# Performance work log

Hardware: AMD Instinct MI355X
Metric: run time of the kernel (lower is better)

## Reference

```python
import jax, jax.numpy as jnp
import numpy as np

N = 65536       # active voxels
C = 128         # embed_channels
DEPTH = 4
NSEG = 1024     # number of clusters per level
K = 27          # 3x3x3 kernel taps
LRELU = 0.01
EPS_BN = 1e-5


def _bn(x, g, b):
    # training-mode batchnorm over the voxel axis (biased variance, as torch)
    m = jnp.mean(x, axis=0)
    v = jnp.var(x, axis=0)
    return (x - m) * jax.lax.rsqrt(v + EPS_BN) * g + b


def _lrelu(x):
    return jnp.where(x >= 0, x, LRELU * x)


def _proj(x, w, g, b):
    # Linear(bias=False) -> BatchNorm1d -> LeakyReLU
    return _lrelu(_bn(x @ w, g, b))


def setup_inputs() -> dict:
    key = jax.random.key(0)
    ks = jax.random.split(key, 24)
    s = 1.0 / np.sqrt(C)
    sc = 1.0 / np.sqrt(K * C)
    u = lambda k, shp, sk: jax.random.uniform(k, shp, jnp.float32, -sk, sk)
    g = lambda k, shp: 1.0 + 0.1 * jax.random.normal(k, shp, jnp.float32)
    inp = {}
    inp['feat'] = jax.random.normal(ks[0], (N, C), jnp.float32)
    inp['clusters'] = jax.random.randint(ks[1], (DEPTH - 1, N), 0, NSEG)
    # neighbor table for 3x3x3 sparse conv; value == N means neighbor absent
    inp['neighbor_idx'] = jax.random.randint(ks[2], (N, K), 0, N + 1)
    inp['lw_w'] = u(ks[3], (DEPTH - 1, C, C), s)
    inp['lw_gamma'] = g(ks[4], (DEPTH - 1, C))
    inp['lw_beta'] = 0.1 * jax.random.normal(ks[5], (DEPTH - 1, C), jnp.float32)
    inp['w_w'] = u(ks[6], (DEPTH - 1, C, C), s)
    inp['proj_w'] = u(ks[7], (DEPTH, C, C), s)
    inp['proj_gamma'] = g(ks[8], (DEPTH, C))
    inp['proj_beta'] = 0.1 * jax.random.normal(ks[9], (DEPTH, C), jnp.float32)
    inp['adaptive_w'] = u(ks[10], (C, DEPTH - 1), s)
    inp['fuse_w'] = u(ks[11], (2 * C, C), 1.0 / np.sqrt(2 * C))
    inp['fuse_gamma'] = g(ks[12], (C,))
    inp['fuse_beta'] = 0.1 * jax.random.normal(ks[13], (C,), jnp.float32)
    inp['conv1_w'] = u(ks[14], (K, C, C), sc)
    inp['conv2_w'] = u(ks[15], (K, C, C), sc)
    inp['bn1_gamma'] = g(ks[16], (C,))
    inp['bn1_beta'] = 0.1 * jax.random.normal(ks[17], (C,), jnp.float32)
    inp['bn2_gamma'] = g(ks[18], (C,))
    inp['bn2_beta'] = 0.1 * jax.random.normal(ks[19], (C,), jnp.float32)
    return inp


def _forward(feat, clusters, neighbor_idx, lw_w, lw_gamma, lw_beta, w_w,
             proj_w, proj_gamma, proj_beta, adaptive_w, fuse_w, fuse_gamma,
             fuse_beta, conv1_w, conv2_w, bn1_gamma, bn1_beta, bn2_gamma,
             bn2_beta):
    x_in = feat
    feats = []
    for i in range(DEPTH - 1):
        c = clusters[i]
        pw = _proj(feat, lw_w[i], lw_gamma[i], lw_beta[i])          # [N,C]
        cnt = jnp.maximum(
            jax.ops.segment_sum(jnp.ones((N,), feat.dtype), c, num_segments=NSEG), 1.0)
        seg_mean = jax.ops.segment_sum(pw, c, num_segments=NSEG) / cnt[:, None]
        pw = pw - seg_mean[c]                                        # center per cluster
        pw = pw @ w_w[i]
        pw = jnp.exp(pw - jnp.max(pw))                               # global max, as in source
        pw = pw / (jax.ops.segment_sum(pw, c, num_segments=NSEG)[c] + 1e-6)
        pf = _proj(feat, proj_w[i], proj_gamma[i], proj_beta[i]) * pw
        feats.append(jax.ops.segment_sum(pf, c, num_segments=NSEG)[c])
    adp = jax.nn.softmax(feat @ adaptive_w, axis=1)                  # [N,3]
    feats = jnp.stack(feats, axis=1)                                 # [N,3,C]
    agg = jnp.einsum('ld,ldc->lc', adp, feats)                       # [N,C]
    f_last = _proj(feat, proj_w[DEPTH - 1], proj_gamma[DEPTH - 1], proj_beta[DEPTH - 1])
    fused = _proj(jnp.concatenate([f_last, agg], axis=1), fuse_w, fuse_gamma, fuse_beta) + x_in
    residual = fused
    # 3x3x3 sparse conv on fixed topology: 27 masked gathers + per-tap GEMM
    mask = (neighbor_idx < N).astype(fused.dtype)                    # [N,K]
    idx = jnp.minimum(neighbor_idx, N - 1)

    def sconv(x, w):
        out = jnp.zeros((N, C), x.dtype)
        for k in range(K):
            out = out + (jnp.take(x, idx[:, k], axis=0) * mask[:, k:k + 1]) @ w[k]
        return out

    d = _lrelu(_bn(sconv(fused, conv1_w), bn1_gamma, bn1_beta))
    d = _lrelu(_bn(sconv(d, conv2_w), bn2_gamma, bn2_beta) + residual)
    return d


def reference(feat, clusters, neighbor_idx, lw_w, lw_gamma, lw_beta, w_w,
              proj_w, proj_gamma, proj_beta, adaptive_w, fuse_w, fuse_gamma,
              fuse_beta, conv1_w, conv2_w, bn1_gamma, bn1_beta, bn2_gamma,
              bn2_beta):
    return _forward(feat, clusters, neighbor_idx, lw_w, lw_gamma, lw_beta,
                    w_w, proj_w, proj_gamma, proj_beta, adaptive_w, fuse_w,
                    fuse_gamma, fuse_beta, conv1_w, conv2_w, bn1_gamma,
                    bn1_beta, bn2_gamma, bn2_beta)
```

## Files before the change

kernel.cpp:

```cpp
#include <hip/hip_runtime.h>

typedef unsigned short u16;
typedef unsigned int u32;
typedef __attribute__((ext_vector_type(8))) short bf16x8;
typedef __attribute__((ext_vector_type(4))) float f32x4;
typedef __attribute__((ext_vector_type(4))) u32 u32x4;

#define NROWS 65536
#define CCH 128
#define PE ((size_t)65537*128)

__device__ __forceinline__ float bf2f(u16 x){ u32 u=((u32)x)<<16; return __builtin_bit_cast(float,u); }
__device__ __forceinline__ u16 f2bf(float f){ u32 u=__builtin_bit_cast(u32,f); u += 0x7fffu + ((u>>16)&1u); return (u16)(u>>16); }
__device__ __forceinline__ float lrelu(float v){ return v>=0.f? v : 0.01f*v; }
__device__ __forceinline__ u32 fenc(float f){ u32 u=__builtin_bit_cast(u32,f); return (u & 0x80000000u) ? ~u : (u | 0x80000000u); }
__device__ __forceinline__ float fdec(u32 u){ u32 b = (u & 0x80000000u) ? (u ^ 0x80000000u) : ~u; return __builtin_bit_cast(float,b); }

__global__ __launch_bounds__(256) void prep_transpose(
    const float* __restrict__ lw, const float* __restrict__ ww, const float* __restrict__ pj,
    const float* __restrict__ fw, const float* __restrict__ c1, const float* __restrict__ c2,
    u16* __restrict__ WT)
{
  int i = blockIdx.x*256 + threadIdx.x;
  float v;
  if (i < 49152)      { int j=i;        int m=j>>14,e=j&16383,n=e>>7,k=e&127; v=lw[(m<<14)+(k<<7)+n]; }
  else if (i < 98304) { int j=i-49152;  int m=j>>14,e=j&16383,n=e>>7,k=e&127; v=ww[(m<<14)+(k<<7)+n]; }
  else if (i < 163840){ int j=i-98304;  int m=j>>14,e=j&16383,n=e>>7,k=e&127; v=pj[(m<<14)+(k<<7)+n]; }
  else if (i < 196608){ int j=i-163840; int n=j>>8, k=j&255;                  v=fw[(k<<7)+n]; }
  else if (i < 638976){ int j=i-196608; int m=j>>14,e=j&16383,n=e>>7,k=e&127; v=c1[(m<<14)+(k<<7)+n]; }
  else                { int j=i-638976; int m=j>>14,e=j&16383,n=e>>7,k=e&127; v=c2[(m<<14)+(k<<7)+n]; }
  WT[i]=f2bf(v);
}

__global__ __launch_bounds__(256) void nbrT_k(const int* __restrict__ nbr, int* __restrict__ nbrT){
  __shared__ int s[64*27];
  int b = blockIdx.x;
  for (int i=threadIdx.x; i<64*27; i+=256) s[i] = nbr[b*64*27 + i];
  __syncthreads();
  for (int i=threadIdx.x; i<64*27; i+=256){
    int tap=i>>6, row=i&63;
    nbrT[(size_t)tap*NROWS + b*64 + row] = s[row*27 + tap];
  }
}

__global__ __launch_bounds__(256) void hist_k(const int* __restrict__ cl, int* __restrict__ cnt){
  int i = blockIdx.x*256 + threadIdx.x;
  int l = i>>16;
  atomicAdd(&cnt[l*1024 + cl[i]], 1);
}
__global__ __launch_bounds__(1024) void scan_k(const int* __restrict__ cnt, int* __restrict__ starts, int* __restrict__ cur){
  int l = blockIdx.x, t = threadIdx.x;
  __shared__ int s[1024];
  int v = cnt[l*1024+t];
  s[t]=v; __syncthreads();
  for (int off=1; off<1024; off<<=1){
    int u_ = (t>=off) ? s[t-off] : 0;
    __syncthreads();
    s[t] += u_;
    __syncthreads();
  }
  int incl=s[t], excl=incl-v;
  starts[l*1025+t]=excl;
  if (t==1023) starts[l*1025+1024]=incl;
  cur[l*1024+t]=excl;
}
__global__ __launch_bounds__(256) void scatter_k(const int* __restrict__ cl, int* __restrict__ cur, int* __restrict__ order){
  int i = blockIdx.x*256 + threadIdx.x;
  int l = i>>16;
  int c = cl[i];
  int p = atomicAdd(&cur[l*1024+c], 1);
  order[l*65536 + p] = i & 65535;
}

struct BS7 { const u16* BT[7]; u16* out[7]; float* stats[7]; };

__global__ __launch_bounds__(256,2) void gemm_feat7(const float* __restrict__ feat, BS7 p)
{
  const int tid=threadIdx.x, lane=tid&63, quad=lane>>4, l15=lane&15;
  const int w=tid>>6, rh=w>>1, chq=w&1;
  const int row0=blockIdx.x*128;

  __shared__ __align__(16) u16 ldsA[128*136];
  __shared__ float cs[256];

  #pragma unroll
  for (int it=0; it<8; ++it){
    int row = it*16 + (tid>>4), chn = tid&15;
    const float* Af = feat + (size_t)(row0+row)*CCH + chn*8;
    float4 lo = *(const float4*)(Af);
    float4 hi = *(const float4*)(Af+4);
    u32x4 d;
    d[0]=(u32)f2bf(lo.x)|((u32)f2bf(lo.y)<<16);
    d[1]=(u32)f2bf(lo.z)|((u32)f2bf(lo.w)<<16);
    d[2]=(u32)f2bf(hi.x)|((u32)f2bf(hi.y)<<16);
    d[3]=(u32)f2bf(hi.z)|((u32)f2bf(hi.w)<<16);
    *(u32x4*)(&ldsA[row*136 + chn*8]) = d;
  }
  __syncthreads();

  #pragma unroll 1
  for (int y=0; y<7; ++y){
    const u16* Bb = p.BT[y];
    f32x4 acc[4][4];
    #pragma unroll
    for (int a_=0;a_<4;++a_)
      #pragma unroll
      for (int b_=0;b_<4;++b_) acc[a_][b_]=(f32x4){0.f,0.f,0.f,0.f};
    #pragma unroll
    for (int ks=0; ks<4; ++ks){
      bf16x8 af[4], bfv[4];
      #pragma unroll
      for (int mb=0;mb<4;++mb)
        af[mb]=*(const bf16x8*)(&ldsA[(rh*64+mb*16+l15)*136 + ks*32 + quad*8]);
      #pragma unroll
      for (int nb=0;nb<4;++nb)
        bfv[nb]=*(const bf16x8*)(Bb + (size_t)(chq*64+nb*16+l15)*CCH + ks*32 + quad*8);
      #pragma unroll
      for (int mb=0;mb<4;++mb)
        #pragma unroll
        for (int nb=0;nb<4;++nb)
          acc[mb][nb]=__builtin_amdgcn_mfma_f32_16x16x32_bf16(af[mb],bfv[nb],acc[mb][nb],0,0,0);
    }
    u16* O = p.out[y];
    #pragma unroll
    for (int mb=0;mb<4;++mb){
      int rbase=row0+rh*64+mb*16+quad*4;
      #pragma unroll
      for (int e=0;e<4;++e)
        #pragma unroll
        for (int nb=0;nb<4;++nb)
          O[(size_t)(rbase+e)*CCH + chq*64+nb*16+l15]=f2bf(acc[mb][nb][e]);
    }
    __syncthreads();
    cs[tid]=0.f;
    __syncthreads();
    #pragma unroll
    for (int nb=0;nb<4;++nb){
      float s=0.f,s2=0.f;
      #pragma unroll
      for (int mb=0;mb<4;++mb)
        #pragma unroll
        for (int e=0;e<4;++e){ float v=acc[mb][nb][e]; s+=v; s2+=v*v; }
      s += __shfl_xor(s,16);  s += __shfl_xor(s,32);
      s2+= __shfl_xor(s2,16); s2+= __shfl_xor(s2,32);
      if (lane<16){
        int col=chq*64+nb*16+l15;
        atomicAdd(&cs[col],s); atomicAdd(&cs[128+col],s2);
      }
    }
    __syncthreads();
    atomicAdd(&p.stats[y][tid], cs[tid]);
  }
}

struct BS3 { const u16* A[3]; const u16* BT[3]; float* out[3]; u32* gmax[3]; };

__global__ __launch_bounds__(256,2) void gemm_w3(BS3 p)
{
  const int tid=threadIdx.x, lane=tid&63, quad=lane>>4, l15=lane&15;
  const int w=tid>>6, rh=w>>1, chq=w&1;
  const int row0=blockIdx.x*128;
  const int y=blockIdx.y;

  __shared__ __align__(16) u16 ldsA[128*136];
  __shared__ float wred[4];

  const u16* A = p.A[y];
  #pragma unroll
  for (int it=0; it<8; ++it){
    int row = it*16 + (tid>>4), chn = tid&15;
    *(u32x4*)(&ldsA[row*136 + chn*8]) = *(const u32x4*)(A + (size_t)(row0+row)*CCH + chn*8);
  }
  __syncthreads();

  const u16* Bb = p.BT[y];
  f32x4 acc[4][4];
  #pragma unroll
  for (int a_=0;a_<4;++a_)
    #pragma unroll
    for (int b_=0;b_<4;++b_) acc[a_][b_]=(f32x4){0.f,0.f,0.f,0.f};
  #pragma unroll
  for (int ks=0; ks<4; ++ks){
    bf16x8 af[4], bfv[4];
    #pragma unroll
    for (int mb=0;mb<4;++mb)
      af[mb]=*(const bf16x8*)(&ldsA[(rh*64+mb*16+l15)*136 + ks*32 + quad*8]);
    #pragma unroll
    for (int nb=0;nb<4;++nb)
      bfv[nb]=*(const bf16x8*)(Bb + (size_t)(chq*64+nb*16+l15)*CCH + ks*32 + quad*8);
    #pragma unroll
    for (int mb=0;mb<4;++mb)
      #pragma unroll
      for (int nb=0;nb<4;++nb)
        acc[mb][nb]=__builtin_amdgcn_mfma_f32_16x16x32_bf16(af[mb],bfv[nb],acc[mb][nb],0,0,0);
  }
  float* O = p.out[y];
  float m=-3.0e38f;
  #pragma unroll
  for (int mb=0;mb<4;++mb){
    int rbase=row0+rh*64+mb*16+quad*4;
    #pragma unroll
    for (int e=0;e<4;++e)
      #pragma unroll
      for (int nb=0;nb<4;++nb){
        float v=acc[mb][nb][e];
        O[(size_t)(rbase+e)*CCH + chq*64+nb*16+l15]=v;
        m=fmaxf(m,v);
      }
  }
  #pragma unroll
  for (int o=1;o<64;o<<=1) m=fmaxf(m,__shfl_xor(m,o));
  if (lane==0) wred[w]=m;
  __syncthreads();
  if (tid==0){
    float mm=fmaxf(fmaxf(wred[0],wred[1]),fmaxf(wred[2],wred[3]));
    atomicMax(p.gmax[y], fenc(mm));
  }
}

__global__ __launch_bounds__(256,2) void gemm_fuse(
    const u16* __restrict__ A0, const u16* __restrict__ A1,
    const float* __restrict__ tstat, const float* __restrict__ tg, const float* __restrict__ tb,
    const u16* __restrict__ BT, u16* __restrict__ out, float* __restrict__ stats)
{
  const int tid=threadIdx.x, lane=tid&63, quad=lane>>4, l15=lane&15;
  const int w=tid>>6, rh=w>>1, chq=w&1;
  const int row0=blockIdx.x*128;

  __shared__ __align__(16) u16 ldsA[128*136];
  __shared__ float tsc[128], tsh[128];
  __shared__ float cs[256];

  if (tid<128){
    float s=tstat[tid], s2=tstat[128+tid];
    float mean=s*(1.0f/65536.0f);
    float var =s2*(1.0f/65536.0f)-mean*mean;
    float rstd=rsqrtf(var+1e-5f);
    float scv =tg[tid]*rstd;
    tsc[tid]=scv; tsh[tid]=tb[tid]-mean*scv;
  }

  f32x4 acc[4][4];
  #pragma unroll
  for (int a_=0;a_<4;++a_)
    #pragma unroll
    for (int b_=0;b_<4;++b_) acc[a_][b_]=(f32x4){0.f,0.f,0.f,0.f};

  #pragma unroll 1
  for (int tap=0; tap<2; ++tap){
    __syncthreads();
    const u16* Ab = tap ? A1 : A0;
    #pragma unroll
    for (int it=0; it<8; ++it){
      int row = it*16 + (tid>>4), chn = tid&15;
      u32x4 d = *(const u32x4*)(Ab + (size_t)(row0+row)*CCH + chn*8);
      if (tap==0){
        #pragma unroll
        for (int pq=0;pq<4;++pq){
          u32 xv=d[pq]; int k=chn*8+2*pq;
          float f0=lrelu(tsc[k  ]*bf2f((u16)(xv&0xffffu))+tsh[k  ]);
          float f1=lrelu(tsc[k+1]*bf2f((u16)(xv>>16))    +tsh[k+1]);
          d[pq]=(u32)f2bf(f0)|((u32)f2bf(f1)<<16);
        }
      }
      *(u32x4*)(&ldsA[row*136 + chn*8]) = d;
    }
    __syncthreads();
    const u16* Bb = BT + tap*128;
    #pragma unroll
    for (int ks=0; ks<4; ++ks){
      bf16x8 af[4], bfv[4];
      #pragma unroll
      for (int mb=0;mb<4;++mb)
        af[mb]=*(const bf16x8*)(&ldsA[(rh*64+mb*16+l15)*136 + ks*32 + quad*8]);
      #pragma unroll
      for (int nb=0;nb<4;++nb)
        bfv[nb]=*(const bf16x8*)(Bb + (size_t)(chq*64+nb*16+l15)*256 + ks*32 + quad*8);
      #pragma unroll
      for (int mb=0;mb<4;++mb)
        #pragma unroll
        for (int nb=0;nb<4;++nb)
          acc[mb][nb]=__builtin_amdgcn_mfma_f32_16x16x32_bf16(af[mb],bfv[nb],acc[mb][nb],0,0,0);
    }
  }
  #pragma unroll
  for (int mb=0;mb<4;++mb){
    int rbase=row0+rh*64+mb*16+quad*4;
    #pragma unroll
    for (int e=0;e<4;++e)
      #pragma unroll
      for (int nb=0;nb<4;++nb)
        out[(size_t)(rbase+e)*CCH + chq*64+nb*16+l15]=f2bf(acc[mb][nb][e]);
  }
  __syncthreads();
  cs[tid]=0.f;
  __syncthreads();
  #pragma unroll
  for (int nb=0;nb<4;++nb){
    float s=0.f,s2=0.f;
    #pragma unroll
    for (int mb=0;mb<4;++mb)
      #pragma unroll
      for (int e=0;e<4;++e){ float v=acc[mb][nb][e]; s+=v; s2+=v*v; }
    s += __shfl_xor(s,16);  s += __shfl_xor(s,32);
    s2+= __shfl_xor(s2,16); s2+= __shfl_xor(s2,32);
    if (lane<16){
      int col=chq*64+nb*16+l15;
      atomicAdd(&cs[col],s); atomicAdd(&cs[128+col],s2);
    }
  }
  __syncthreads();
  atomicAdd(&stats[tid], cs[tid]);
}

__global__ __launch_bounds__(256,2) void conv_k(
    const u16* __restrict__ A, const u16* __restrict__ BT,
    const int* __restrict__ nbrT, u16* __restrict__ out, float* __restrict__ stats)
{
  const int tid=threadIdx.x, lane=tid&63, quad=lane>>4, l15=lane&15;
  const int w=tid>>6, rh=w>>1, chq=w&1;
  const int row0=blockIdx.x*128;
  const int srow=tid>>4, schn=tid&15;

  __shared__ __align__(16) u16 bufA[2][128*136];
  __shared__ float cs[256];

  u32x4 pre[8];
  int idxn[8];
  #pragma unroll
  for (int it=0; it<8; ++it){
    int arow = nbrT[row0 + it*16 + srow];
    pre[it] = *(const u32x4*)(A + (size_t)arow*CCH + schn*8);
  }
  #pragma unroll
  for (int it=0; it<8; ++it)
    idxn[it] = nbrT[(size_t)NROWS + row0 + it*16 + srow];
  #pragma unroll
  for (int it=0; it<8; ++it)
    *(u32x4*)(&bufA[0][(it*16+srow)*136 + schn*8]) = pre[it];
  __syncthreads();

  f32x4 acc[4][4];
  #pragma unroll
  for (int a_=0;a_<4;++a_)
    #pragma unroll
    for (int b_=0;b_<4;++b_) acc[a_][b_]=(f32x4){0.f,0.f,0.f,0.f};

  #pragma unroll 1
  for (int tap=0; tap<27; ++tap){
    const int cur = tap&1, nxt = cur^1;
    if (tap<26){
      #pragma unroll
      for (int it=0; it<8; ++it)
        pre[it] = *(const u32x4*)(A + (size_t)idxn[it]*CCH + schn*8);
      if (tap<25){
        #pragma unroll
        for (int it=0; it<8; ++it)
          idxn[it] = nbrT[(size_t)(tap+2)*NROWS + row0 + it*16 + srow];
      }
    }
    const u16* Bb = BT + tap*16384;
    #pragma unroll
    for (int ks=0; ks<4; ++ks){
      bf16x8 af[4], bfv[4];
      #pragma unroll
      for (int mb=0;mb<4;++mb)
        af[mb]=*(const bf16x8*)(&bufA[cur][(rh*64+mb*16+l15)*136 + ks*32 + quad*8]);
      #pragma unroll
      for (int nb=0;nb<4;++nb)
        bfv[nb]=*(const bf16x8*)(Bb + (size_t)(chq*64+nb*16+l15)*CCH + ks*32 + quad*8);
      #pragma unroll
      for (int mb=0;mb<4;++mb)
        #pragma unroll
        for (int nb=0;nb<4;++nb)
          acc[mb][nb]=__builtin_amdgcn_mfma_f32_16x16x32_bf16(af[mb],bfv[nb],acc[mb][nb],0,0,0);
    }
    if (tap<26){
      #pragma unroll
      for (int it=0; it<8; ++it)
        *(u32x4*)(&bufA[nxt][(it*16+srow)*136 + schn*8]) = pre[it];
    }
    __syncthreads();
  }

  #pragma unroll
  for (int mb=0;mb<4;++mb){
    int rbase=row0+rh*64+mb*16+quad*4;
    #pragma unroll
    for (int e=0;e<4;++e)
      #pragma unroll
      for (int nb=0;nb<4;++nb)
        out[(size_t)(rbase+e)*CCH + chq*64+nb*16+l15]=f2bf(acc[mb][nb][e]);
  }
  cs[tid]=0.f;
  __syncthreads();
  #pragma unroll
  for (int nb=0;nb<4;++nb){
    float s=0.f,s2=0.f;
    #pragma unroll
    for (int mb=0;mb<4;++mb)
      #pragma unroll
      for (int e=0;e<4;++e){ float v=acc[mb][nb][e]; s+=v; s2+=v*v; }
    s += __shfl_xor(s,16);  s += __shfl_xor(s,32);
    s2+= __shfl_xor(s2,16); s2+= __shfl_xor(s2,32);
    if (lane<16){
      int col=chq*64+nb*16+l15;
      atomicAdd(&cs[col],s); atomicAdd(&cs[128+col],s2);
    }
  }
  __syncthreads();
  atomicAdd(&stats[tid], cs[tid]);
}

__global__ __launch_bounds__(256) void seg_bn_center_all(
    u16* __restrict__ pbase, const float* __restrict__ stats,
    const float* __restrict__ gamma, const float* __restrict__ beta,
    const int* __restrict__ starts, const int* __restrict__ order)
{
  __shared__ float sc[128], sh[128], ssum[128], smean[128];
  const int tid=threadIdx.x, b=blockIdx.x;
  const int level=b>>10, seg=b&1023;
  u16* praw = pbase + (size_t)level*PE;
  const float* st = stats + level*256;
  if (tid<128){
    float s=st[tid], s2=st[128+tid];
    float mean=s*(1.0f/65536.0f);
    float var =s2*(1.0f/65536.0f)-mean*mean;
    float rstd=rsqrtf(var+1e-5f);
    float scv =gamma[level*128+tid]*rstd;
    sc[tid]=scv; sh[tid]=beta[level*128+tid]-mean*scv;
    ssum[tid]=0.f;
  }
  __syncthreads();
  const int s0=starts[level*1025+seg], en=starts[level*1025+seg+1];
  const int c2=tid&63, half=tid>>6;
  const int* ord = order + level*65536;
  const float sc0=sc[2*c2], sc1=sc[2*c2+1], sh0=sh[2*c2], sh1=sh[2*c2+1];
  float a0=0.f, a1=0.f;
  for (int m=s0+half; m<en; m+=4){
    int r=ord[m];
    u32 x=*(const u32*)(praw + (size_t)r*CCH + 2*c2);
    a0 += lrelu(sc0*bf2f((u16)(x&0xffffu))+sh0);
    a1 += lrelu(sc1*bf2f((u16)(x>>16))    +sh1);
  }
  atomicAdd(&ssum[2*c2],a0); atomicAdd(&ssum[2*c2+1],a1);
  __syncthreads();
  if (tid<128) smean[tid]=ssum[tid]/fmaxf((float)(en-s0),1.0f);
  __syncthreads();
  const float m0=smean[2*c2], m1=smean[2*c2+1];
  for (int m=s0+half; m<en; m+=4){
    int r=ord[m];
    u32 x=*(const u32*)(praw + (size_t)r*CCH + 2*c2);
    float v0=lrelu(sc0*bf2f((u16)(x&0xffffu))+sh0)-m0;
    float v1=lrelu(sc1*bf2f((u16)(x>>16))    +sh1)-m1;
    *(u32*)(praw + (size_t)r*CCH + 2*c2) = (u32)f2bf(v0)|((u32)f2bf(v1)<<16);
  }
}

struct F3 { const float* f[3]; };
__global__ __launch_bounds__(256) void seg_softmax_all(
    F3 pw2s, const u16* __restrict__ pfbase,
    const float* __restrict__ stats, const float* __restrict__ gamma, const float* __restrict__ beta,
    const u32* __restrict__ gmax,
    const int* __restrict__ starts, const int* __restrict__ order,
    float* __restrict__ segpf)
{
  __shared__ float sc[128], sh[128], se[128], spf[128];
  const int tid=threadIdx.x, b=blockIdx.x;
  const int level=b>>10, seg=b&1023;
  const float* pw2 = pw2s.f[level];
  const u16* pfraw = pfbase + (size_t)level*PE;
  const float* st = stats + level*256;
  if (tid<128){
    float s=st[tid], s2=st[128+tid];
    float mean=s*(1.0f/65536.0f);
    float var =s2*(1.0f/65536.0f)-mean*mean;
    float rstd=rsqrtf(var+1e-5f);
    float scv =gamma[level*128+tid]*rstd;
    sc[tid]=scv; sh[tid]=beta[level*128+tid]-mean*scv;
    se[tid]=0.f; spf[tid]=0.f;
  }
  __syncthreads();
  const float M = fdec(gmax[level]);
  const int s0=starts[level*1025+seg], en=starts[level*1025+seg+1];
  const int c2=tid&63, half=tid>>6;
  const int* ord = order + level*65536;
  float a0=0.f, a1=0.f;
  for (int m=s0+half; m<en; m+=4){
    int r=ord[m];
    float2 x=*(const float2*)(pw2 + (size_t)r*CCH + 2*c2);
    a0 += __expf(x.x-M); a1 += __expf(x.y-M);
  }
  atomicAdd(&se[2*c2],a0); atomicAdd(&se[2*c2+1],a1);
  __syncthreads();
  const float d0=1.0f/(se[2*c2]+1e-6f), d1=1.0f/(se[2*c2+1]+1e-6f);
  const float sc0=sc[2*c2], sc1=sc[2*c2+1], sh0=sh[2*c2], sh1=sh[2*c2+1];
  float p0=0.f, p1=0.f;
  for (int m=s0+half; m<en; m+=4){
    int r=ord[m];
    float2 x=*(const float2*)(pw2 + (size_t)r*CCH + 2*c2);
    u32 f=*(const u32*)(pfraw + (size_t)r*CCH + 2*c2);
    p0 += lrelu(sc0*bf2f((u16)(f&0xffffu))+sh0) * (__expf(x.x-M)*d0);
    p1 += lrelu(sc1*bf2f((u16)(f>>16))    +sh1) * (__expf(x.y-M)*d1);
  }
  atomicAdd(&spf[2*c2],p0); atomicAdd(&spf[2*c2+1],p1);
  __syncthreads();
  if (tid<128) segpf[(size_t)b*128+tid]=spf[tid];
}

__global__ __launch_bounds__(256) void adp_agg(
    const float* __restrict__ feat, const float* __restrict__ aw,
    const int* __restrict__ clusters, const float* __restrict__ segpf,
    u16* __restrict__ agg)
{
  const int tid=threadIdx.x, w=tid>>6, lane=tid&63;
  const int r = blockIdx.x*4 + w;
  float t0=0.f,t1=0.f,t2=0.f;
  #pragma unroll
  for (int cc=0; cc<2; ++cc){
    int c = lane + cc*64;
    float f=feat[(size_t)r*CCH+c];
    t0 += f*aw[c*3+0];
    t1 += f*aw[c*3+1];
    t2 += f*aw[c*3+2];
  }
  #pragma unroll
  for (int o=1;o<64;o<<=1){
    t0+=__shfl_xor(t0,o); t1+=__shfl_xor(t1,o); t2+=__shfl_xor(t2,o);
  }
  float m=fmaxf(t0,fmaxf(t1,t2));
  float e0=__expf(t0-m), e1=__expf(t1-m), e2=__expf(t2-m);
  float inv=1.0f/(e0+e1+e2);
  float p0=e0*inv,p1=e1*inv,p2=e2*inv;
  int c0=clusters[r], c1_=clusters[NROWS+r], c2_=clusters[2*NROWS+r];
  const float* s0p=segpf + (size_t)c0*128;
  const float* s1p=segpf + (size_t)(1024+c1_)*128;
  const float* s2p=segpf + (size_t)(2048+c2_)*128;
  #pragma unroll
  for (int cc=0; cc<2; ++cc){
    int c = lane + cc*64;
    float v = p0*s0p[c] + p1*s1p[c] + p2*s2p[c];
    agg[(size_t)r*CCH+c]=f2bf(v);
  }
}

__global__ __launch_bounds__(256) void apply_kernel(
    const u16* __restrict__ raw, const float* __restrict__ stats,
    const float* __restrict__ g_, const float* __restrict__ b_,
    const void* __restrict__ resid, int rf32,
    void* __restrict__ out, int of32,
    int nrows, int mode)
{
  __shared__ float sc[128], sh[128];
  const int tid=threadIdx.x;
  if (tid<128){
    float s=stats[tid], s2=stats[128+tid];
    float mean=s*(1.0f/65536.0f);
    float var =s2*(1.0f/65536.0f)-mean*mean;
    float rstd=rsqrtf(var+1e-5f);
    float scv =g_[tid]*rstd;
    sc[tid]=scv; sh[tid]=b_[tid]-mean*scv;
  }
  __syncthreads();
  size_t chunk = (size_t)blockIdx.x*256 + tid;
  size_t total = (size_t)nrows*16;
  if (chunk >= total) return;
  size_t r = chunk>>4; int c8 = (int)(chunk&15)*8;
  float v[8];
  if (r >= NROWS){
    #pragma unroll
    for (int p=0;p<8;++p) v[p]=0.f;
  } else {
    u32x4 x = *(const u32x4*)(raw + r*CCH + c8);
    float rsd[8];
    if (resid){
      if (rf32){
        const float* R = ((const float*)resid) + r*CCH + c8;
        float4 lo=*(const float4*)R, hi=*(const float4*)(R+4);
        rsd[0]=lo.x; rsd[1]=lo.y; rsd[2]=lo.z; rsd[3]=lo.w;
        rsd[4]=hi.x; rsd[5]=hi.y; rsd[6]=hi.z; rsd[7]=hi.w;
      } else {
        u32x4 rv = *(const u32x4*)(((const u16*)resid) + r*CCH + c8);
        #pragma unroll
        for (int p=0;p<4;++p){
          rsd[2*p]  =bf2f((u16)(rv[p]&0xffffu));
          rsd[2*p+1]=bf2f((u16)(rv[p]>>16));
        }
      }
    } else {
      #pragma unroll
      for (int p=0;p<8;++p) rsd[p]=0.f;
    }
    #pragma unroll
    for (int p=0;p<4;++p){
      u32 xv=x[p];
      int k=c8+2*p;
      float v0=sc[k  ]*bf2f((u16)(xv&0xffffu))+sh[k  ];
      float v1=sc[k+1]*bf2f((u16)(xv>>16))    +sh[k+1];
      if (mode==0){ v[2*p]=lrelu(v0)+rsd[2*p]; v[2*p+1]=lrelu(v1)+rsd[2*p+1]; }
      else        { v[2*p]=lrelu(v0+rsd[2*p]); v[2*p+1]=lrelu(v1+rsd[2*p+1]); }
    }
  }
  if (of32){
    float* O = ((float*)out) + r*CCH + c8;
    float4 lo={v[0],v[1],v[2],v[3]}, hi={v[4],v[5],v[6],v[7]};
    *(float4*)O = lo; *(float4*)(O+4) = hi;
  } else {
    u32x4 o;
    #pragma unroll
    for (int p=0;p<4;++p) o[p] = (u32)f2bf(v[2*p]) | ((u32)f2bf(v[2*p+1])<<16);
    *(u32x4*)(((u16*)out) + r*CCH + c8) = o;
  }
}

extern "C" void kernel_launch(void* const* d_in, const int* in_sizes, int n_in,
                              void* d_out, int out_size, void* d_ws, size_t ws_size,
                              hipStream_t stream)
{
  (void)in_sizes; (void)n_in; (void)out_size; (void)ws_size;
  const float* feat = (const float*)d_in[0];
  const int* clusters = (const int*)d_in[1];
  const int* nbr  = (const int*)d_in[2];
  const float* lw_w = (const float*)d_in[3];
  const float* lw_g = (const float*)d_in[4];
  const float* lw_b = (const float*)d_in[5];
  const float* w_w  = (const float*)d_in[6];
  const float* pj_w = (const float*)d_in[7];
  const float* pj_g = (const float*)d_in[8];
  const float* pj_b = (const float*)d_in[9];
  const float* aw   = (const float*)d_in[10];
  const float* fu_w = (const float*)d_in[11];
  const float* fu_g = (const float*)d_in[12];
  const float* fu_b = (const float*)d_in[13];
  const float* c1w  = (const float*)d_in[14];
  const float* c2w  = (const float*)d_in[15];
  const float* b1g  = (const float*)d_in[16];
  const float* b1b  = (const float*)d_in[17];
  const float* b2g  = (const float*)d_in[18];
  const float* b2b  = (const float*)d_in[19];

  char* wsb = (char*)d_ws;
  u16* WT = (u16*)wsb;
  const size_t o_zero = 2162688;
  float* stats = (float*)(wsb + o_zero);
  u32*  gmax   = (u32*) (wsb + o_zero + 10240);
  int*  cnt    = (int*) (wsb + o_zero + 10496);
  int*  cur    = (int*) (wsb + o_zero + 22784);
  float* segpf = (float*)(wsb + o_zero + 35072);
  const size_t zero_bytes = 35072 + (size_t)3*1024*128*4;
  const size_t o_starts = o_zero + 1607936;
  int* starts = (int*)(wsb + o_starts);
  const size_t o_order = o_starts + 12544;
  int* order  = (int*)(wsb + o_order);
  const size_t o_pool = o_order + 786432;
  const size_t PE_B = PE*2;
  u16* A0=(u16*)(wsb+o_pool + 0*PE_B);
  u16* A1=(u16*)(wsb+o_pool + 1*PE_B);
  u16* A2=(u16*)(wsb+o_pool + 2*PE_B);
  u16* A3=(u16*)(wsb+o_pool + 3*PE_B);
  u16* A4=(u16*)(wsb+o_pool + 4*PE_B);
  u16* A5=(u16*)(wsb+o_pool + 5*PE_B);
  u16* A6=(u16*)(wsb+o_pool + 6*PE_B);
  const size_t o_F = o_pool + 7*PE_B;
  float* F0=(float*)(wsb+o_F);
  float* F1=(float*)(wsb+o_F+33554432);
  float* F2=(float*)d_out;
  int* nbrT = (int*)(wsb+o_F);

  hipMemsetAsync(wsb+o_zero, 0, zero_bytes, stream);
  prep_transpose<<<4224,256,0,stream>>>(lw_w,w_w,pj_w,fu_w,c1w,c2w,WT);
  hist_k   <<<768,256,0,stream>>>(clusters, cnt);
  scan_k   <<<3,1024,0,stream>>>(cnt, starts, cur);
  scatter_k<<<768,256,0,stream>>>(clusters, cur, order);

  const u16* lwT = WT;
  const u16* wwT = WT + 49152;
  const u16* pjT = WT + 98304;
  const u16* fuT = WT + 163840;
  const u16* c1T = WT + 196608;
  const u16* c2T = WT + 638976;

  float* stLW=stats;
  float* stPJ=stats+768;
  float* stFU=stats+1792; float* stB1=stats+2048; float* stB2=stats+2304;

  {
    BS7 p;
    for (int i=0;i<3;++i){ p.BT[i]=lwT+i*16384;     p.out[i]=A0+(size_t)i*PE; p.stats[i]=stLW+i*256; }
    for (int i=0;i<4;++i){ p.BT[3+i]=pjT+i*16384;   p.out[3+i]=(i<3)?(A3+(size_t)i*PE):A6; p.stats[3+i]=stPJ+i*256; }
    gemm_feat7<<<512,256,0,stream>>>(feat, p);
  }
  seg_bn_center_all<<<3072,256,0,stream>>>(A0, stLW, lw_g, lw_b, starts, order);
  {
    BS3 p;
    float* Fo[3]={F0,F1,F2};
    for (int i=0;i<3;++i){ p.A[i]=A0+(size_t)i*PE; p.BT[i]=wwT+i*16384; p.out[i]=Fo[i]; p.gmax[i]=gmax+i; }
    gemm_w3<<<dim3(512,3),256,0,stream>>>(p);
  }
  {
    F3 f; f.f[0]=F0; f.f[1]=F1; f.f[2]=F2;
    seg_softmax_all<<<3072,256,0,stream>>>(f, A3, stPJ, pj_g, pj_b, gmax, starts, order, segpf);
  }
  nbrT_k<<<1024,256,0,stream>>>(nbr, nbrT);
  adp_agg<<<16384,256,0,stream>>>(feat, aw, clusters, segpf, A4);
  gemm_fuse<<<512,256,0,stream>>>(A6, A4, stPJ+768, pj_g+384, pj_b+384, fuT, A5, stFU);
  apply_kernel<<<4097,256,0,stream>>>(A5, stFU, fu_g, fu_b, feat, 1, A0, 0, NROWS+1, 0);
  conv_k<<<512,256,0,stream>>>(A0, c1T, nbrT, A1, stB1);
  apply_kernel<<<4097,256,0,stream>>>(A1, stB1, b1g, b1b, nullptr, 0, A2, 0, NROWS+1, 0);
  conv_k<<<512,256,0,stream>>>(A2, c2T, nbrT, A3, stB2);
  apply_kernel<<<4096,256,0,stream>>>(A3, stB2, b2g, b2b, A0, 0, (float*)d_out, 1, NROWS, 1);
}
```

Before: 724.5 us.

## Fuse segment centering into logits GEMM, store logits as bf16, merge prep kernels

Changes seg_bn_center_all so it only computes per-segment means (seg_sum_all). The BN+lrelu+mean subtraction now happens inside the logits GEMM's A-tile load, which removes a second gather pass and an in-place scattered write. The logits GEMM writes bf16 instead of fp32, halving its output traffic and the softmax reads, at some precision cost in the exp. The histogram is folded into prep_transpose and the scatter into the neighbor transpose kernel, which cuts launch count. The memset also shrinks because segpf no longer needs zeroing.

New measurement: 699.0 us. 1.04x faster.

```diff
diff --git a/kernel.cpp b/kernel.cpp
--- a/kernel.cpp
+++ b/kernel.cpp
@@ -19,7 +19,7 @@
 __global__ __launch_bounds__(256) void prep_transpose(
     const float* __restrict__ lw, const float* __restrict__ ww, const float* __restrict__ pj,
     const float* __restrict__ fw, const float* __restrict__ c1, const float* __restrict__ c2,
-    u16* __restrict__ WT)
+    u16* __restrict__ WT, const int* __restrict__ cl, int* __restrict__ cnt)
 {
   int i = blockIdx.x*256 + threadIdx.x;
   float v;
@@ -30,24 +30,9 @@
   else if (i < 638976){ int j=i-196608; int m=j>>14,e=j&16383,n=e>>7,k=e&127; v=c1[(m<<14)+(k<<7)+n]; }
   else                { int j=i-638976; int m=j>>14,e=j&16383,n=e>>7,k=e&127; v=c2[(m<<14)+(k<<7)+n]; }
   WT[i]=f2bf(v);
-}
-
-__global__ __launch_bounds__(256) void nbrT_k(const int* __restrict__ nbr, int* __restrict__ nbrT){
-  __shared__ int s[64*27];
-  int b = blockIdx.x;
-  for (int i=threadIdx.x; i<64*27; i+=256) s[i] = nbr[b*64*27 + i];
-  __syncthreads();
-  for (int i=threadIdx.x; i<64*27; i+=256){
-    int tap=i>>6, row=i&63;
-    nbrT[(size_t)tap*NROWS + b*64 + row] = s[row*27 + tap];
-  }
-}
-
-__global__ __launch_bounds__(256) void hist_k(const int* __restrict__ cl, int* __restrict__ cnt){
-  int i = blockIdx.x*256 + threadIdx.x;
-  int l = i>>16;
-  atomicAdd(&cnt[l*1024 + cl[i]], 1);
-}
+  if (i < 196608) atomicAdd(&cnt[(i>>16)*1024 + cl[i]], 1);
+}
+
 __global__ __launch_bounds__(1024) void scan_k(const int* __restrict__ cnt, int* __restrict__ starts, int* __restrict__ cur){
   int l = blockIdx.x, t = threadIdx.x;
   __shared__ int s[1024];
@@ -64,12 +49,26 @@
   if (t==1023) starts[l*1025+1024]=incl;
   cur[l*1024+t]=excl;
 }
-__global__ __launch_bounds__(256) void scatter_k(const int* __restrict__ cl, int* __restrict__ cur, int* __restrict__ order){
-  int i = blockIdx.x*256 + threadIdx.x;
-  int l = i>>16;
-  int c = cl[i];
-  int p = atomicAdd(&cur[l*1024+c], 1);
-  order[l*65536 + p] = i & 65535;
+
+__global__ __launch_bounds__(256) void scatter_nbrT(
+    const int* __restrict__ cl, int* __restrict__ cur, int* __restrict__ order,
+    const int* __restrict__ nbr, int* __restrict__ nbrT)
+{
+  __shared__ int s[64*27];
+  const int b = blockIdx.x, tid = threadIdx.x;
+  int i = b*256 + tid;
+  if (i < 196608){
+    int l = i>>16;
+    int c = cl[i];
+    int p = atomicAdd(&cur[l*1024+c], 1);
+    order[l*65536 + p] = i & 65535;
+  }
+  for (int j=tid; j<64*27; j+=256) s[j] = nbr[b*64*27 + j];
+  __syncthreads();
+  for (int j=tid; j<64*27; j+=256){
+    int tap=j>>6, row=j&63;
+    nbrT[(size_t)tap*NROWS + b*64 + row] = s[row*27 + tap];
+  }
 }
 
 struct BS7 { const u16* BT[7]; u16* out[7]; float* stats[7]; };
@@ -153,9 +152,52 @@
   }
 }
 
-struct BS3 { const u16* A[3]; const u16* BT[3]; float* out[3]; u32* gmax[3]; };
-
-__global__ __launch_bounds__(256,2) void gemm_w3(BS3 p)
+__global__ __launch_bounds__(256) void seg_sum_all(
+    const u16* __restrict__ pbase, const float* __restrict__ stats,
+    const float* __restrict__ gamma, const float* __restrict__ beta,
+    const int* __restrict__ starts, const int* __restrict__ order,
+    u16* __restrict__ segmean)
+{
+  __shared__ float sc[128], sh[128], ssum[128];
+  const int tid=threadIdx.x, b=blockIdx.x;
+  const int level=b>>10, seg=b&1023;
+  const u16* praw = pbase + (size_t)level*PE;
+  const float* st = stats + level*256;
+  if (tid<128){
+    float s=st[tid], s2=st[128+tid];
+    float mean=s*(1.0f/65536.0f);
+    float var =s2*(1.0f/65536.0f)-mean*mean;
+    float rstd=rsqrtf(var+1e-5f);
+    float scv =gamma[level*128+tid]*rstd;
+    sc[tid]=scv; sh[tid]=beta[level*128+tid]-mean*scv;
+    ssum[tid]=0.f;
+  }
+  __syncthreads();
+  const int s0=starts[level*1025+seg], en=starts[level*1025+seg+1];
+  const int c2=tid&63, half=tid>>6;
+  const int* ord = order + level*65536;
+  const float sc0=sc[2*c2], sc1=sc[2*c2+1], sh0=sh[2*c2], sh1=sh[2*c2+1];
+  float a0=0.f, a1=0.f;
+  for (int m=s0+half; m<en; m+=4){
+    int r=ord[m];
+    u32 x=*(const u32*)(praw + (size_t)r*CCH + 2*c2);
+    a0 += lrelu(sc0*bf2f((u16)(x&0xffffu))+sh0);
+    a1 += lrelu(sc1*bf2f((u16)(x>>16))    +sh1);
+  }
+  atomicAdd(&ssum[2*c2],a0); atomicAdd(&ssum[2*c2+1],a1);
+  __syncthreads();
+  if (tid<128){
+    float inv = 1.0f/fmaxf((float)(en-s0),1.0f);
+    segmean[(size_t)b*128+tid]=f2bf(ssum[tid]*inv);
+  }
+}
+
+struct LG { const u16* A[3]; u16* out[3]; };
+__global__ __launch_bounds__(256,2) void gemm_logits(
+    LG p, const u16* __restrict__ wwT,
+    const float* __restrict__ stats, const float* __restrict__ lwg, const float* __restrict__ lwb,
+    const int* __restrict__ clusters, const u16* __restrict__ segmean,
+    u32* __restrict__ gmax)
 {
   const int tid=threadIdx.x, lane=tid&63, quad=lane>>4, l15=lane&15;
   const int w=tid>>6, rh=w>>1, chq=w&1;
@@ -163,17 +205,40 @@
   const int y=blockIdx.y;
 
   __shared__ __align__(16) u16 ldsA[128*136];
+  __shared__ float tsc[128], tsh[128];
   __shared__ float wred[4];
 
-  const u16* A = p.A[y];
+  if (tid<128){
+    const float* st = stats + y*256;
+    float s=st[tid], s2=st[128+tid];
+    float mean=s*(1.0f/65536.0f);
+    float var =s2*(1.0f/65536.0f)-mean*mean;
+    float rstd=rsqrtf(var+1e-5f);
+    float scv =lwg[y*128+tid]*rstd;
+    tsc[tid]=scv; tsh[tid]=lwb[y*128+tid]-mean*scv;
+  }
+  __syncthreads();
+
+  const u16* Ab = p.A[y];
+  const u16* smb = segmean + (size_t)y*1024*128;
   #pragma unroll
   for (int it=0; it<8; ++it){
     int row = it*16 + (tid>>4), chn = tid&15;
-    *(u32x4*)(&ldsA[row*136 + chn*8]) = *(const u32x4*)(A + (size_t)(row0+row)*CCH + chn*8);
-  }
-  __syncthreads();
-
-  const u16* Bb = p.BT[y];
+    int cl = clusters[(size_t)y*NROWS + row0 + row];
+    u32x4 d  = *(const u32x4*)(Ab + (size_t)(row0+row)*CCH + chn*8);
+    u32x4 sm = *(const u32x4*)(smb + (size_t)cl*CCH + chn*8);
+    #pragma unroll
+    for (int pq=0;pq<4;++pq){
+      u32 xv=d[pq], sv=sm[pq]; int k=chn*8+2*pq;
+      float f0=lrelu(tsc[k  ]*bf2f((u16)(xv&0xffffu))+tsh[k  ]) - bf2f((u16)(sv&0xffffu));
+      float f1=lrelu(tsc[k+1]*bf2f((u16)(xv>>16))    +tsh[k+1]) - bf2f((u16)(sv>>16));
+      d[pq]=(u32)f2bf(f0)|((u32)f2bf(f1)<<16);
+    }
+    *(u32x4*)(&ldsA[row*136 + chn*8]) = d;
+  }
+  __syncthreads();
+
+  const u16* Bb = wwT + y*16384;
   f32x4 acc[4][4];
   #pragma unroll
   for (int a_=0;a_<4;++a_)
@@ -194,19 +259,21 @@
       for (int nb=0;nb<4;++nb)
         acc[mb][nb]=__builtin_amdgcn_mfma_f32_16x16x32_bf16(af[mb],bfv[nb],acc[mb][nb],0,0,0);
   }
-  float* O = p.out[y];
+  u16* O = p.out[y];
   float m=-3.0e38f;
   #pragma unroll
   for (int mb=0;mb<4;++mb){
     int rbase=row0+rh*64+mb*16+quad*4;
     #pragma unroll
-    for (int e=0;e<4;++e)
+    for (int e=0;e<4;++e){
+      int row=rbase+e;
       #pragma unroll
       for (int nb=0;nb<4;++nb){
-        float v=acc[mb][nb][e];
-        O[(size_t)(rbase+e)*CCH + chq*64+nb*16+l15]=v;
-        m=fmaxf(m,v);
+        u16 rv = f2bf(acc[mb][nb][e]);
+        O[(size_t)row*CCH + chq*64+nb*16+l15]=rv;
+        m=fmaxf(m,bf2f(rv));
       }
+    }
   }
   #pragma unroll
   for (int o=1;o<64;o<<=1) m=fmaxf(m,__shfl_xor(m,o));
@@ -214,7 +281,7 @@
   __syncthreads();
   if (tid==0){
     float mm=fmaxf(fmaxf(wred[0],wred[1]),fmaxf(wred[2],wred[3]));
-    atomicMax(p.gmax[y], fenc(mm));
+    atomicMax(&gmax[y], fenc(mm));
   }
 }
 
@@ -412,52 +479,7 @@
   atomicAdd(&stats[tid], cs[tid]);
 }
 
-__global__ __launch_bounds__(256) void seg_bn_center_all(
-    u16* __restrict__ pbase, const float* __restrict__ stats,
-    const float* __restrict__ gamma, const float* __restrict__ beta,
-    const int* __restrict__ starts, const int* __restrict__ order)
-{
-  __shared__ float sc[128], sh[128], ssum[128], smean[128];
-  const int tid=threadIdx.x, b=blockIdx.x;
-  const int level=b>>10, seg=b&1023;
-  u16* praw = pbase + (size_t)level*PE;
-  const float* st = stats + level*256;
-  if (tid<128){
-    float s=st[tid], s2=st[128+tid];
-    float mean=s*(1.0f/65536.0f);
-    float var =s2*(1.0f/65536.0f)-mean*mean;
-    float rstd=rsqrtf(var+1e-5f);
-    float scv =gamma[level*128+tid]*rstd;
-    sc[tid]=scv; sh[tid]=beta[level*128+tid]-mean*scv;
-    ssum[tid]=0.f;
-  }
-  __syncthreads();
-  const int s0=starts[level*1025+seg], en=starts[level*1025+seg+1];
-  const int c2=tid&63, half=tid>>6;
-  const int* ord = order + level*65536;
-  const float sc0=sc[2*c2], sc1=sc[2*c2+1], sh0=sh[2*c2], sh1=sh[2*c2+1];
-  float a0=0.f, a1=0.f;
-  for (int m=s0+half; m<en; m+=4){
-    int r=ord[m];
-    u32 x=*(const u32*)(praw + (size_t)r*CCH + 2*c2);
-    a0 += lrelu(sc0*bf2f((u16)(x&0xffffu))+sh0);
-    a1 += lrelu(sc1*bf2f((u16)(x>>16))    +sh1);
-  }
-  atomicAdd(&ssum[2*c2],a0); atomicAdd(&ssum[2*c2+1],a1);
-  __syncthreads();
-  if (tid<128) smean[tid]=ssum[tid]/fmaxf((float)(en-s0),1.0f);
-  __syncthreads();
-  const float m0=smean[2*c2], m1=smean[2*c2+1];
-  for (int m=s0+half; m<en; m+=4){
-    int r=ord[m];
-    u32 x=*(const u32*)(praw + (size_t)r*CCH + 2*c2);
-    float v0=lrelu(sc0*bf2f((u16)(x&0xffffu))+sh0)-m0;
-    float v1=lrelu(sc1*bf2f((u16)(x>>16))    +sh1)-m1;
-    *(u32*)(praw + (size_t)r*CCH + 2*c2) = (u32)f2bf(v0)|((u32)f2bf(v1)<<16);
-  }
-}
-
-struct F3 { const float* f[3]; };
+struct F3 { const u16* f[3]; };
 __global__ __launch_bounds__(256) void seg_softmax_all(
     F3 pw2s, const u16* __restrict__ pfbase,
     const float* __restrict__ stats, const float* __restrict__ gamma, const float* __restrict__ beta,
@@ -468,7 +490,7 @@
   __shared__ float sc[128], sh[128], se[128], spf[128];
   const int tid=threadIdx.x, b=blockIdx.x;
   const int level=b>>10, seg=b&1023;
-  const float* pw2 = pw2s.f[level];
+  const u16* pw2 = pw2s.f[level];
   const u16* pfraw = pfbase + (size_t)level*PE;
   const float* st = stats + level*256;
   if (tid<128){
@@ -488,8 +510,9 @@
   float a0=0.f, a1=0.f;
   for (int m=s0+half; m<en; m+=4){
     int r=ord[m];
-    float2 x=*(const float2*)(pw2 + (size_t)r*CCH + 2*c2);
-    a0 += __expf(x.x-M); a1 += __expf(x.y-M);
+    u32 x=*(const u32*)(pw2 + (size_t)r*CCH + 2*c2);
+    a0 += __expf(bf2f((u16)(x&0xffffu))-M);
+    a1 += __expf(bf2f((u16)(x>>16))   -M);
   }
   atomicAdd(&se[2*c2],a0); atomicAdd(&se[2*c2+1],a1);
   __syncthreads();
@@ -498,10 +521,10 @@
   float p0=0.f, p1=0.f;
   for (int m=s0+half; m<en; m+=4){
     int r=ord[m];
-    float2 x=*(const float2*)(pw2 + (size_t)r*CCH + 2*c2);
+    u32 x=*(const u32*)(pw2 + (size_t)r*CCH + 2*c2);
     u32 f=*(const u32*)(pfraw + (size_t)r*CCH + 2*c2);
-    p0 += lrelu(sc0*bf2f((u16)(f&0xffffu))+sh0) * (__expf(x.x-M)*d0);
-    p1 += lrelu(sc1*bf2f((u16)(f>>16))    +sh1) * (__expf(x.y-M)*d1);
+    p0 += lrelu(sc0*bf2f((u16)(f&0xffffu))+sh0) * (__expf(bf2f((u16)(x&0xffffu))-M)*d0);
+    p1 += lrelu(sc1*bf2f((u16)(f>>16))    +sh1) * (__expf(bf2f((u16)(x>>16))   -M)*d1);
   }
   atomicAdd(&spf[2*c2],p0); atomicAdd(&spf[2*c2+1],p1);
   __syncthreads();
@@ -645,10 +668,11 @@
   float* stats = (float*)(wsb + o_zero);
   u32*  gmax   = (u32*) (wsb + o_zero + 10240);
   int*  cnt    = (int*) (wsb + o_zero + 10496);
+  const size_t zero_bytes = 22784;
   int*  cur    = (int*) (wsb + o_zero + 22784);
-  float* segpf = (float*)(wsb + o_zero + 35072);
-  const size_t zero_bytes = 35072 + (size_t)3*1024*128*4;
-  const size_t o_starts = o_zero + 1607936;
+  u16*  segmean= (u16*) (wsb + o_zero + 35072);
+  float* segpf = (float*)(wsb + o_zero + 821504);
+  const size_t o_starts = o_zero + 2394368;
   int* starts = (int*)(wsb + o_starts);
   const size_t o_order = o_starts + 12544;
   int* order  = (int*)(wsb + o_order);
@@ -662,16 +686,15 @@
   u16* A5=(u16*)(wsb+o_pool + 5*PE_B);
   u16* A6=(u16*)(wsb+o_pool + 6*PE_B);
   const size_t o_F = o_pool + 7*PE_B;
-  float* F0=(float*)(wsb+o_F);
-  float* F1=(float*)(wsb+o_F+33554432);
-  float* F2=(float*)d_out;
-  int* nbrT = (int*)(wsb+o_F);
+  u16* F0=(u16*)(wsb+o_F);
+  u16* F1=(u16*)(wsb+o_F+PE_B);
+  u16* F2=(u16*)d_out;
+  int* nbrT = (int*)(wsb+o_F+2*PE_B);
 
   hipMemsetAsync(wsb+o_zero, 0, zero_bytes, stream);
-  prep_transpose<<<4224,256,0,stream>>>(lw_w,w_w,pj_w,fu_w,c1w,c2w,WT);
-  hist_k   <<<768,256,0,stream>>>(clusters, cnt);
-  scan_k   <<<3,1024,0,stream>>>(cnt, starts, cur);
-  scatter_k<<<768,256,0,stream>>>(clusters, cur, order);
+  prep_transpose<<<4224,256,0,stream>>>(lw_w,w_w,pj_w,fu_w,c1w,c2w,WT, clusters, cnt);
+  scan_k<<<3,1024,0,stream>>>(cnt, starts, cur);
+  scatter_nbrT<<<1024,256,0,stream>>>(clusters, cur, order, nbr, nbrT);
 
   const u16* lwT = WT;
   const u16* wwT = WT + 49152;
@@ -690,18 +713,17 @@
     for (int i=0;i<4;++i){ p.BT[3+i]=pjT+i*16384;   p.out[3+i]=(i<3)?(A3+(size_t)i*PE):A6; p.stats[3+i]=stPJ+i*256; }
     gemm_feat7<<<512,256,0,stream>>>(feat, p);
   }
-  seg_bn_center_all<<<3072,256,0,stream>>>(A0, stLW, lw_g, lw_b, starts, order);
+  seg_sum_all<<<3072,256,0,stream>>>(A0, stLW, lw_g, lw_b, starts, order, segmean);
   {
-    BS3 p;
-    float* Fo[3]={F0,F1,F2};
-    for (int i=0;i<3;++i){ p.A[i]=A0+(size_t)i*PE; p.BT[i]=wwT+i*16384; p.out[i]=Fo[i]; p.gmax[i]=gmax+i; }
-    gemm_w3<<<dim3(512,3),256,0,stream>>>(p);
+    LG p;
+    u16* Fo[3]={F0,F1,F2};
+    for (int i=0;i<3;++i){ p.A[i]=A0+(size_t)i*PE; p.out[i]=Fo[i]; }
+    gemm_logits<<<dim3(512,3),256,0,stream>>>(p, wwT, stLW, lw_g, lw_b, clusters, segmean, gmax);
   }
   {
     F3 f; f.f[0]=F0; f.f[1]=F1; f.f[2]=F2;
     seg_softmax_all<<<3072,256,0,stream>>>(f, A3, stPJ, pj_g, pj_b, gmax, starts, order, segpf);
   }
-  nbrT_k<<<1024,256,0,stream>>>(nbr, nbrT);
   adp_agg<<<16384,256,0,stream>>>(feat, aw, clusters, segpf, A4);
   gemm_fuse<<<512,256,0,stream>>>(A6, A4, stPJ+768, pj_g+384, pj_b+384, fuT, A5, stFU);
   apply_kernel<<<4097,256,0,stream>>>(A5, stFU, fu_g, fu_b, feat, 1, A0, 0, NROWS+1, 0);
```
